# Kernel optimization log

Hardware: AMD Instinct MI355X
Metric: run time of the kernel (lower is better)

Reference implementation:

```python
import jax, jax.numpy as jnp
import numpy as np

B, N, C = 32, 577, 768
H = 12
D = C // H


def setup_inputs() -> dict:
    key = jax.random.key(0)
    ks = jax.random.split(key, 4)
    x = jax.random.normal(ks[0], (B, N, C), dtype=jnp.float32)
    w_qkv = jax.random.normal(ks[1], (C, 3 * C), dtype=jnp.float32) * (C ** -0.5)
    b_qkv = jnp.zeros((3 * C,), dtype=jnp.float32)
    # per-head learnable scale, initialized to head_dim**-0.5 scaled ones
    scale = jnp.ones((H,), dtype=jnp.float32) * (D ** -0.5)
    w_proj = jax.random.normal(ks[2], (C, C), dtype=jnp.float32) * (C ** -0.5)
    b_proj = jnp.zeros((C,), dtype=jnp.float32)
    return {"x": x, "w_qkv": w_qkv, "b_qkv": b_qkv, "scale": scale,
            "w_proj": w_proj, "b_proj": b_proj}


def reference(x, w_qkv, b_qkv, scale, w_proj, b_proj):
    b, n, c = x.shape
    h = scale.shape[0]
    d = c // h
    # fused QKV projection -> [b, n, 3, h, d]
    qkv = (x @ w_qkv + b_qkv).reshape(b, n, 3, h, d)
    q = qkv[:, :, 0]  # [b, n, h, d]
    k = qkv[:, :, 1]
    v = qkv[:, :, 2]
    # attention logits with per-head scale
    attn = jnp.einsum('bihd,bjhd->bhij', q, k) * scale[None, :, None, None]
    # custom mask: block self-attention among patch tokens (rows/cols 1:),
    # CLS token (index 0) unaffected
    if n > 1:
        mask = jnp.zeros((n, n), dtype=bool).at[1:, 1:].set(
            jnp.eye(n - 1, dtype=bool))
        attn = jnp.where(mask[None, None], -jnp.inf, attn)
    attn = jax.nn.softmax(attn, axis=-1)
    out = jnp.einsum('bhij,bjhd->bihd', attn, v).reshape(b, n, c)
    return out @ w_proj + b_proj
```

## Files before the change

kernel.cpp:

```cpp
#include <hip/hip_runtime.h>
#include <math.h>

#define HD 64
#define KVBLK 64
#define LP 72

typedef __attribute__((ext_vector_type(8))) short short8;
typedef __attribute__((ext_vector_type(4))) short short4v;
typedef __attribute__((ext_vector_type(4))) float f32x4;

__device__ __forceinline__ short f2bf(float f) {
    union { float f; unsigned u; } in;
    in.f = f;
    unsigned r = (in.u + 0x7fff + ((in.u >> 16) & 1)) >> 16;
    return (short)r;
}

__global__ __launch_bounds__(256) void convert_bf16(const float* __restrict__ in,
                                                    short* __restrict__ out, long n4) {
    long i = blockIdx.x * 256L + threadIdx.x;
    if (i >= n4) return;
    float4 v = reinterpret_cast<const float4*>(in)[i];
    short4v o;
    o[0] = f2bf(v.x); o[1] = f2bf(v.y); o[2] = f2bf(v.z); o[3] = f2bf(v.w);
    reinterpret_cast<short4v*>(out)[i] = o;
}

__global__ __launch_bounds__(256) void transpose_bf16(const float* __restrict__ in,
                                                      short* __restrict__ out, int K, int N) {
    __shared__ float tile[32][33];
    const int n0 = blockIdx.x * 32, k0 = blockIdx.y * 32;
    const int tx = threadIdx.x & 31, ty = threadIdx.x >> 5;
    #pragma unroll
    for (int i = ty; i < 32; i += 8)
        tile[i][tx] = in[(size_t)(k0 + i) * N + n0 + tx];
    __syncthreads();
    #pragma unroll
    for (int i = ty; i < 32; i += 8)
        out[(size_t)(n0 + i) * K + k0 + tx] = f2bf(tile[tx][i]);
}

__global__ __launch_bounds__(256) void transpose_v(const short* __restrict__ qkvb,
                                                   short* __restrict__ vT) {
    constexpr int Nn = 577, C3 = 2304, NH = 12, NKP = 640;
    const int bh = blockIdx.x;
    const int kt = blockIdx.y;
    const int b = bh / NH, h = bh % NH;
    const int tid = threadIdx.x;
    __shared__ short tile[64][33];

    const int tk = tid >> 3;
    const int key = kt * 32 + tk;
    const int d0 = (tid & 7) * 8;
    short8 v = {0, 0, 0, 0, 0, 0, 0, 0};
    if (key < Nn)
        v = *reinterpret_cast<const short8*>(
            qkvb + (size_t)(b * Nn + key) * C3 + 1536 + h * 64 + d0);
    #pragma unroll
    for (int i = 0; i < 8; ++i) tile[d0 + i][tk] = v[i];
    __syncthreads();

    const int d = tid >> 2;
    const int kb = (tid & 3) * 8;
    short8 o;
    #pragma unroll
    for (int i = 0; i < 8; ++i) o[i] = tile[d][kb + i];
    *reinterpret_cast<short8*>(vT + (size_t)(bh * 64 + d) * NKP + kt * 32 + kb) = o;
}

template <typename OutT>
__global__ __launch_bounds__(256) void gemm_bf16(const short* __restrict__ A,
                                                 const short* __restrict__ Bt,
                                                 const float* __restrict__ bias,
                                                 OutT* __restrict__ C,
                                                 int M, int N, int K, int nbn) {
    __shared__ short As[2][128 * 64];
    __shared__ short Bs[2][128 * 64];
    const int tid = threadIdx.x;
    const int w = tid >> 6, lane = tid & 63;
    const int g = lane >> 4, l16 = lane & 15;

    const int nwg = gridDim.x;
    const int q = nwg >> 3, r = nwg & 7;
    const int xcd = blockIdx.x & 7, loc = blockIdx.x >> 3;
    const int wgid = (xcd < r ? xcd * (q + 1) : r * (q + 1) + (xcd - r) * q) + loc;
    const int bm = wgid / nbn, bn = wgid % nbn;
    const int m0 = bm * 128, n0 = bn * 128;
    const int wm = (w >> 1) * 64, wn = (w & 1) * 64;

    f32x4 acc[4][4] = {};

    const int lr = lane >> 3;
    const int lc = (lane & 7) * 8;
    const int NT = K >> 6;

    auto stage = [&](int buf, int k0) {
        #pragma unroll
        for (int t = 0; t < 4; ++t) {
            const int rr = 32 * w + 8 * t + lr;
            long arow = m0 + rr; if (arow > M - 1) arow = M - 1;
            const short* ga = A + arow * K + k0 + lc;
            const short* gb = Bt + (size_t)(n0 + rr) * K + k0 + lc;
            __builtin_amdgcn_global_load_lds(
                (const __attribute__((address_space(1))) unsigned*)ga,
                (__attribute__((address_space(3))) unsigned*)&As[buf][(32 * w + 8 * t) * 64],
                16, 0, 0);
            __builtin_amdgcn_global_load_lds(
                (const __attribute__((address_space(1))) unsigned*)gb,
                (__attribute__((address_space(3))) unsigned*)&Bs[buf][(32 * w + 8 * t) * 64],
                16, 0, 0);
        }
    };

    stage(0, 0);
    __syncthreads();

    for (int kt = 0; kt < NT; ++kt) {
        const int cur = kt & 1;
        if (kt + 1 < NT) stage(cur ^ 1, (kt + 1) * 64);

        #pragma unroll
        for (int ks = 0; ks < 2; ++ks) {
            short8 af[4], bfr[4];
            #pragma unroll
            for (int mi = 0; mi < 4; ++mi)
                af[mi] = *reinterpret_cast<const short8*>(
                    &As[cur][(wm + mi * 16 + l16) * 64 + ks * 32 + g * 8]);
            #pragma unroll
            for (int ni = 0; ni < 4; ++ni)
                bfr[ni] = *reinterpret_cast<const short8*>(
                    &Bs[cur][(wn + ni * 16 + l16) * 64 + ks * 32 + g * 8]);
            __builtin_amdgcn_s_setprio(1);
            #pragma unroll
            for (int mi = 0; mi < 4; ++mi)
                #pragma unroll
                for (int ni = 0; ni < 4; ++ni)
                    acc[mi][ni] = __builtin_amdgcn_mfma_f32_16x16x32_bf16(
                        af[mi], bfr[ni], acc[mi][ni], 0, 0, 0);
            __builtin_amdgcn_s_setprio(0);
        }
        __syncthreads();
    }

    float bv[4];
    #pragma unroll
    for (int ni = 0; ni < 4; ++ni) bv[ni] = bias[n0 + wn + ni * 16 + l16];
    #pragma unroll
    for (int mi = 0; mi < 4; ++mi) {
        #pragma unroll
        for (int rr = 0; rr < 4; ++rr) {
            const int row = m0 + wm + mi * 16 + g * 4 + rr;
            if (row < M) {
                #pragma unroll
                for (int ni = 0; ni < 4; ++ni) {
                    float val = acc[mi][ni][rr] + bv[ni];
                    if constexpr (__is_same(OutT, float))
                        C[(size_t)row * N + n0 + wn + ni * 16 + l16] = val;
                    else
                        C[(size_t)row * N + n0 + wn + ni * 16 + l16] = f2bf(val);
                }
            }
        }
    }
}

__global__ __launch_bounds__(256) void flash_attn(const short* __restrict__ qkvb,
                                                  const short* __restrict__ vT,
                                                  const float* __restrict__ scale,
                                                  short* __restrict__ out) {
    constexpr int Nn = 577, Cc = 768, C3 = 2304, NQB = 10, NH = 12, NT = 10, NKP = 640;
    const int bid = blockIdx.x;
    const int swz = (bid & 7) * 480 + (bid >> 3);
    const int q0 = (swz % NQB) * 64;
    const int h  = (swz / NQB) % NH;
    const int b  = swz / (NQB * NH);
    const int qblk = q0 >> 6;

    const int tid  = threadIdx.x;
    const int w    = tid >> 6;
    const int lane = tid & 63;
    const int g    = lane >> 4;
    const int l16  = lane & 15;

    __shared__ alignas(16) short Ks[2][KVBLK * HD];
    __shared__ alignas(16) short Vts[2][HD * KVBLK];
    __shared__ alignas(16) short Ps[4][16][LP];
    __shared__ float facs[4][16];

    const float sl2 = scale[h] * 1.44269504088896f;
    const float thr = 8.0f / sl2;
    const short* base = qkvb + (size_t)b * Nn * C3;
    const short* kglob = base + Cc + h * HD;
    const short* vtb = vT + (size_t)(b * NH + h) * HD * NKP;

    const int qrow = q0 + w * 16 + l16;
    const int qr = qrow < Nn ? qrow : Nn - 1;
    const short* qp = base + (size_t)qr * C3 + h * HD;
    short8 aq[2];
    aq[0] = *reinterpret_cast<const short8*>(qp + 8 * g);
    aq[1] = *reinterpret_cast<const short8*>(qp + 32 + 8 * g);

    f32x4 oacc[4] = {};
    float mrun = -INFINITY, m2 = -INFINITY, lrun = 0.f;

    const int kst_row = lane >> 3;
    const int kst_dblk = (lane & 7) ^ (lane >> 3);

    auto stageK = [&](int bufi, int kv0) {
        #pragma unroll
        for (int t = 0; t < 2; ++t) {
            const int i = 2 * w + t;
            int kr = kv0 + 8 * i + kst_row;
            if (kr > Nn - 1) kr = Nn - 1;
            const short* src = kglob + (size_t)kr * C3 + kst_dblk * 8;
            __builtin_amdgcn_global_load_lds(
                (const __attribute__((address_space(1))) unsigned*)src,
                (__attribute__((address_space(3))) unsigned*)&Ks[bufi][i * 512],
                16, 0, 0);
        }
    };
    auto stageV = [&](int bufi, int kv0) {
        #pragma unroll
        for (int t = 0; t < 2; ++t) {
            const int i = 2 * w + t;
            const int r = 8 * i + kst_row;
            const int kb = (lane & 7) ^ (r & 7);
            const short* src = vtb + (size_t)r * NKP + kv0 + kb * 8;
            __builtin_amdgcn_global_load_lds(
                (const __attribute__((address_space(1))) unsigned*)src,
                (__attribute__((address_space(3))) unsigned*)&Vts[bufi][i * 512],
                16, 0, 0);
        }
    };

    stageK(0, 0);
    stageV(0, 0);
    __syncthreads();

    for (int t = 0; t < NT; ++t) {
        const int cur = t & 1, nxt = cur ^ 1;
        const int kv0 = t * KVBLK;
        const bool more = (t + 1 < NT);
        if (more) { stageK(nxt, kv0 + KVBLK); stageV(nxt, kv0 + KVBLK); }

        f32x4 sacc[4] = {};
        __builtin_amdgcn_s_setprio(1);
        #pragma unroll
        for (int f = 0; f < 4; ++f) {
            #pragma unroll
            for (int c = 0; c < 2; ++c) {
                const int slot = (4 * c + g) ^ (l16 & 7);
                short8 ak = *reinterpret_cast<const short8*>(
                    &Ks[cur][(16 * f + l16) * 64 + slot * 8]);
                sacc[f] = __builtin_amdgcn_mfma_f32_16x16x32_bf16(ak, aq[c], sacc[f], 0, 0, 0);
            }
        }
        __builtin_amdgcn_s_setprio(0);

        const int ig = q0 + w * 16 + l16;
        float s2[4][4];
        #pragma unroll
        for (int f = 0; f < 4; ++f)
            #pragma unroll
            for (int r = 0; r < 4; ++r)
                s2[f][r] = sacc[f][r];
        if (t == qblk || t == NT - 1) {
            #pragma unroll
            for (int f = 0; f < 4; ++f)
                #pragma unroll
                for (int r = 0; r < 4; ++r) {
                    const int jg = kv0 + 16 * f + 4 * g + r;
                    if (jg >= Nn || (jg == ig && ig >= 1)) s2[f][r] = -INFINITY;
                }
        }

        float mx = s2[0][0];
        #pragma unroll
        for (int f = 0; f < 4; ++f)
            #pragma unroll
            for (int r = 0; r < 4; ++r)
                if (f + r) mx = fmaxf(mx, s2[f][r]);
        mx = fmaxf(mx, __shfl_xor(mx, 16, 64));
        mx = fmaxf(mx, __shfl_xor(mx, 32, 64));

        if (__any(mx > mrun + thr)) {
            const float mnew = fmaxf(mrun, mx);
            const float m2new = mnew * sl2;
            const float fac = __builtin_amdgcn_exp2f(m2 - m2new);
            mrun = mnew; m2 = m2new;
            lrun *= fac;
            if (lane < 16) facs[w][lane] = fac;
            asm volatile("s_waitcnt lgkmcnt(0)" ::: "memory");
            #pragma unroll
            for (int r = 0; r < 4; ++r) {
                const float fr = facs[w][4 * g + r];
                #pragma unroll
                for (int df = 0; df < 4; ++df) oacc[df][r] *= fr;
            }
        }

        float sum = 0.f;
        #pragma unroll
        for (int f = 0; f < 4; ++f)
            #pragma unroll
            for (int r = 0; r < 4; ++r) {
                float p = __builtin_amdgcn_exp2f(fmaf(s2[f][r], sl2, -m2));
                s2[f][r] = p;
                sum += p;
            }
        sum += __shfl_xor(sum, 16, 64);
        sum += __shfl_xor(sum, 32, 64);
        lrun += sum;

        #pragma unroll
        for (int f = 0; f < 4; ++f) {
            unsigned plo, phi;
            asm("v_cvt_pk_bf16_f32 %0, %1, %2" : "=v"(plo) : "v"(s2[f][0]), "v"(s2[f][1]));
            asm("v_cvt_pk_bf16_f32 %0, %1, %2" : "=v"(phi) : "v"(s2[f][2]), "v"(s2[f][3]));
            unsigned* dst = reinterpret_cast<unsigned*>(&Ps[w][l16][16 * f + 4 * g]);
            dst[0] = plo; dst[1] = phi;
        }
        asm volatile("s_waitcnt lgkmcnt(0)" ::: "memory");

        __builtin_amdgcn_s_setprio(1);
        #pragma unroll
        for (int c = 0; c < 2; ++c) {
            short8 pa = *reinterpret_cast<const short8*>(&Ps[w][l16][32 * c + 8 * g]);
            #pragma unroll
            for (int df = 0; df < 4; ++df) {
                const int slot = (4 * c + g) ^ (l16 & 7);
                short8 bv = *reinterpret_cast<const short8*>(
                    &Vts[cur][(16 * df + l16) * 64 + slot * 8]);
                oacc[df] = __builtin_amdgcn_mfma_f32_16x16x32_bf16(pa, bv, oacc[df], 0, 0, 0);
            }
        }
        __builtin_amdgcn_s_setprio(0);
        __syncthreads();
    }

    if (lane < 16) facs[w][lane] = lrun;
    asm volatile("s_waitcnt lgkmcnt(0)" ::: "memory");
    #pragma unroll
    for (int r = 0; r < 4; ++r) {
        const int og = q0 + w * 16 + g * 4 + r;
        if (og < Nn) {
            const float inv = 1.f / facs[w][4 * g + r];
            #pragma unroll
            for (int df = 0; df < 4; ++df)
                out[(size_t)(b * Nn + og) * Cc + h * HD + 16 * df + l16] =
                    f2bf(oacc[df][r] * inv);
        }
    }
}

extern "C" void kernel_launch(void* const* d_in, const int* in_sizes, int n_in,
                              void* d_out, int out_size, void* d_ws, size_t ws_size,
                              hipStream_t stream) {
    const float* x      = (const float*)d_in[0];
    const float* w_qkv  = (const float*)d_in[1];
    const float* b_qkv  = (const float*)d_in[2];
    const float* scale  = (const float*)d_in[3];
    const float* w_proj = (const float*)d_in[4];
    const float* b_proj = (const float*)d_in[5];
    float* out = (float*)d_out;

    const int B = 32, N = 577, C = 768, H = 12;
    const int M  = B * N;
    const int C3 = 3 * C;
    const int MB = (M + 127) / 128;

    short* qkvb   = (short*)d_ws;
    short* attn_o = qkvb + (size_t)M * C3;
    short* xb     = attn_o + (size_t)M * C;
    short* wqkvT  = xb + (size_t)M * C;
    short* wprojT = wqkvT + (size_t)C3 * C;
    short* vT     = wprojT + (size_t)C * C;

    dim3 blk(256);
    const long n4 = (long)M * C / 4;
    convert_bf16<<<dim3((n4 + 255) / 256), blk, 0, stream>>>(x, xb, n4);
    transpose_bf16<<<dim3(C3 / 32, C / 32), blk, 0, stream>>>(w_qkv, wqkvT, C, C3);
    transpose_bf16<<<dim3(C / 32, C / 32), blk, 0, stream>>>(w_proj, wprojT, C, C);

    gemm_bf16<short><<<dim3(MB * (C3 / 128)), blk, 0, stream>>>(
        xb, wqkvT, b_qkv, qkvb, M, C3, C, C3 / 128);

    transpose_v<<<dim3(B * H, 20), blk, 0, stream>>>(qkvb, vT);

    flash_attn<<<dim3(((N + 63) / 64) * H * B), blk, 0, stream>>>(qkvb, vT, scale, attn_o);

    gemm_bf16<float><<<dim3(MB * (C / 128)), blk, 0, stream>>>(
        attn_o, wprojT, b_proj, out, M, C, C, C / 128);
}
```

Measured before the change: 277.1 us.

## Swizzle GEMM LDS layout with K-tile 32 and use shuffles for softmax rescale

The bf16 GEMM now stages K-slices of 32 instead of 64, halving its shared-memory footprint. Its A/B tiles are stored two logical rows per 128-byte LDS row with an XOR swizzle, so the fragment reads avoid bank conflicts. In exchange it runs twice as many k-iterations, each with a barrier. The attention kernel drops the small LDS scratch for the rescale factor and the final row sum and broadcasts them with cross-lane shuffles, removing LDS round-trips and waitcnts.

New measurement: 261.3 us. 5.7% less time.

```diff
diff --git a/kernel.cpp b/kernel.cpp
--- a/kernel.cpp
+++ b/kernel.cpp
@@ -74,8 +74,8 @@
                                                  const float* __restrict__ bias,
                                                  OutT* __restrict__ C,
                                                  int M, int N, int K, int nbn) {
-    __shared__ short As[2][128 * 64];
-    __shared__ short Bs[2][128 * 64];
+    __shared__ short As[2][64 * 64];
+    __shared__ short Bs[2][64 * 64];
     const int tid = threadIdx.x;
     const int w = tid >> 6, lane = tid & 63;
     const int g = lane >> 4, l16 = lane & 15;
@@ -89,25 +89,26 @@
     const int wm = (w >> 1) * 64, wn = (w & 1) * 64;
 
     f32x4 acc[4][4] = {};
-
-    const int lr = lane >> 3;
-    const int lc = (lane & 7) * 8;
-    const int NT = K >> 6;
+    const int NT = K >> 5;
 
     auto stage = [&](int buf, int k0) {
         #pragma unroll
-        for (int t = 0; t < 4; ++t) {
-            const int rr = 32 * w + 8 * t + lr;
+        for (int j = 0; j < 2; ++j) {
+            const int o = j * 4096 + tid * 16;
+            const int R = o >> 7;
+            const int sl = ((o >> 4) & 7) ^ (R & 7);
+            const int rr = 2 * R + (sl >> 2);
+            const int cblk = sl & 3;
             long arow = m0 + rr; if (arow > M - 1) arow = M - 1;
-            const short* ga = A + arow * K + k0 + lc;
-            const short* gb = Bt + (size_t)(n0 + rr) * K + k0 + lc;
+            const short* ga = A + arow * K + k0 + cblk * 8;
+            const short* gb = Bt + (size_t)(n0 + rr) * K + k0 + cblk * 8;
             __builtin_amdgcn_global_load_lds(
                 (const __attribute__((address_space(1))) unsigned*)ga,
-                (__attribute__((address_space(3))) unsigned*)&As[buf][(32 * w + 8 * t) * 64],
+                (__attribute__((address_space(3))) unsigned*)((char*)&As[buf][0] + o),
                 16, 0, 0);
             __builtin_amdgcn_global_load_lds(
                 (const __attribute__((address_space(1))) unsigned*)gb,
-                (__attribute__((address_space(3))) unsigned*)&Bs[buf][(32 * w + 8 * t) * 64],
+                (__attribute__((address_space(3))) unsigned*)((char*)&Bs[buf][0] + o),
                 16, 0, 0);
         }
     };
@@ -117,28 +118,31 @@
 
     for (int kt = 0; kt < NT; ++kt) {
         const int cur = kt & 1;
-        if (kt + 1 < NT) stage(cur ^ 1, (kt + 1) * 64);
-
-        #pragma unroll
-        for (int ks = 0; ks < 2; ++ks) {
-            short8 af[4], bfr[4];
-            #pragma unroll
-            for (int mi = 0; mi < 4; ++mi)
-                af[mi] = *reinterpret_cast<const short8*>(
-                    &As[cur][(wm + mi * 16 + l16) * 64 + ks * 32 + g * 8]);
+        if (kt + 1 < NT) stage(cur ^ 1, (kt + 1) * 32);
+
+        short8 af[4], bfr[4];
+        #pragma unroll
+        for (int mi = 0; mi < 4; ++mi) {
+            const int ra = wm + mi * 16 + l16;
+            const int Ra = ra >> 1;
+            const int sla = (4 * (ra & 1) + g) ^ (Ra & 7);
+            af[mi] = *reinterpret_cast<const short8*>(&As[cur][Ra * 64 + sla * 8]);
+        }
+        #pragma unroll
+        for (int ni = 0; ni < 4; ++ni) {
+            const int rb = wn + ni * 16 + l16;
+            const int Rb = rb >> 1;
+            const int slb = (4 * (rb & 1) + g) ^ (Rb & 7);
+            bfr[ni] = *reinterpret_cast<const short8*>(&Bs[cur][Rb * 64 + slb * 8]);
+        }
+        __builtin_amdgcn_s_setprio(1);
+        #pragma unroll
+        for (int mi = 0; mi < 4; ++mi)
             #pragma unroll
             for (int ni = 0; ni < 4; ++ni)
-                bfr[ni] = *reinterpret_cast<const short8*>(
-                    &Bs[cur][(wn + ni * 16 + l16) * 64 + ks * 32 + g * 8]);
-            __builtin_amdgcn_s_setprio(1);
-            #pragma unroll
-            for (int mi = 0; mi < 4; ++mi)
-                #pragma unroll
-                for (int ni = 0; ni < 4; ++ni)
-                    acc[mi][ni] = __builtin_amdgcn_mfma_f32_16x16x32_bf16(
-                        af[mi], bfr[ni], acc[mi][ni], 0, 0, 0);
-            __builtin_amdgcn_s_setprio(0);
-        }
+                acc[mi][ni] = __builtin_amdgcn_mfma_f32_16x16x32_bf16(
+                    af[mi], bfr[ni], acc[mi][ni], 0, 0, 0);
+        __builtin_amdgcn_s_setprio(0);
         __syncthreads();
     }
 
@@ -185,7 +189,6 @@
     __shared__ alignas(16) short Ks[2][KVBLK * HD];
     __shared__ alignas(16) short Vts[2][HD * KVBLK];
     __shared__ alignas(16) short Ps[4][16][LP];
-    __shared__ float facs[4][16];
 
     const float sl2 = scale[h] * 1.44269504088896f;
     const float thr = 8.0f / sl2;
@@ -289,11 +292,9 @@
             const float fac = __builtin_amdgcn_exp2f(m2 - m2new);
             mrun = mnew; m2 = m2new;
             lrun *= fac;
-            if (lane < 16) facs[w][lane] = fac;
-            asm volatile("s_waitcnt lgkmcnt(0)" ::: "memory");
             #pragma unroll
             for (int r = 0; r < 4; ++r) {
-                const float fr = facs[w][4 * g + r];
+                const float fr = __shfl(fac, 16 * g + 4 * g + r, 64);
                 #pragma unroll
                 for (int df = 0; df < 4; ++df) oacc[df][r] *= fr;
             }
@@ -338,13 +339,12 @@
         __syncthreads();
     }
 
-    if (lane < 16) facs[w][lane] = lrun;
-    asm volatile("s_waitcnt lgkmcnt(0)" ::: "memory");
     #pragma unroll
     for (int r = 0; r < 4; ++r) {
         const int og = q0 + w * 16 + g * 4 + r;
         if (og < Nn) {
-            const float inv = 1.f / facs[w][4 * g + r];
+            const float lr_r = __shfl(lrun, 16 * g + 4 * g + r, 64);
+            const float inv = 1.f / lr_r;
             #pragma unroll
             for (int df = 0; df < 4; ++df)
                 out[(size_t)(b * Nn + og) * Cc + h * HD + 16 * df + l16] =
```
